# Optimization experiments

Hardware: AMD Instinct MI355X
Metric: run time of the kernel (lower is better)

Reference implementation:

```python
import jax, jax.numpy as jnp
import numpy as np

E, T, K, H, I = 16, 512, 8, 2048, 1024  # experts, tokens, top-k, hidden, ffn half-width


def setup_inputs() -> dict:
    key = jax.random.key(0)
    ks = jax.random.split(key, 8)
    x = jax.random.normal(ks[0], (T, H), dtype=jnp.float32)
    expert_ids = jax.random.randint(ks[1], (T, K), 0, E, dtype=jnp.int32)
    # int8-valued weights stored as int32 (exactly representable)
    gmm1_weight = jax.random.randint(ks[2], (E, H, 2 * I), -127, 128, dtype=jnp.int32)
    gmm2_weight = jax.random.randint(ks[3], (E, I, H), -127, 128, dtype=jnp.int32)
    gmm1_weight_scale = jax.random.uniform(ks[4], (E, 2 * I), dtype=jnp.float32) * 1e-3
    gmm2_weight_scale = jax.random.uniform(ks[5], (E, H), dtype=jnp.float32) * 1e-3
    smooth_scales = jax.random.uniform(ks[6], (E, H), dtype=jnp.float32)
    expert_scales = jax.random.uniform(ks[7], (T, K), dtype=jnp.float32)
    return {"x": x, "expert_ids": expert_ids, "gmm1_weight": gmm1_weight,
            "gmm1_weight_scale": gmm1_weight_scale, "gmm2_weight": gmm2_weight,
            "gmm2_weight_scale": gmm2_weight_scale, "smooth_scales": smooth_scales,
            "expert_scales": expert_scales}


def _dynamic_quant(v):
    # per-token symmetric dynamic quant to int8 range (quant_mode=2 / quant_mode=1)
    s = jnp.max(jnp.abs(v), axis=-1, keepdims=True) / 127.0
    q = jnp.clip(jnp.round(v / s), -128.0, 127.0)  # kept in f32; values are exact small ints
    return q, s


def _grouped_mm(a, w, e_flat):
    # grouped GEMM: out[i] = a[i] @ w[e_flat[i]]. Disjoint expert masks -> masked full GEMMs summed.
    out = jnp.zeros((a.shape[0], w.shape[-1]), dtype=a.dtype)
    for e in range(w.shape[0]):
        mask = (e_flat == e)[:, None]
        out = out + jnp.where(mask, a, 0.0) @ w[e]
    return out


def reference(x, expert_ids, gmm1_weight, gmm1_weight_scale, gmm2_weight,
              gmm2_weight_scale, smooth_scales, expert_scales):
    # --- dispatch: per-token dynamic int8 quant + replicate each token K times ---
    xq, s0 = _dynamic_quant(x)                 # [T,H], [T,1]
    e_flat = expert_ids.reshape(-1)            # [T*K]
    xq_e = jnp.repeat(xq, K, axis=0)           # [T*K,H]
    s0_e = jnp.repeat(s0, K, axis=0)           # [T*K,1] == dynamic_scales / activation_scale
    w1 = gmm1_weight.astype(jnp.float32)       # int8 GEMM emulated exactly in f32
    w2 = gmm2_weight.astype(jnp.float32)
    # --- grouped GEMM 1 -> int32 accumulator values ---
    y1_i32 = _grouped_mm(xq_e, w1, e_flat)     # [T*K,2I]
    # --- fused dequant + SwiGLU (activate_left) + per-token dynamic requant ---
    y1f = y1_i32 * gmm1_weight_scale[e_flat] * s0_e
    act = jax.nn.silu(y1f[:, :I]) * y1f[:, I:]
    aq, s1 = _dynamic_quant(act)               # [T*K,I], [T*K,1]
    # --- grouped GEMM 2 + dequant (per-channel weight scale * per-token scale) ---
    y2_i32 = _grouped_mm(aq, w2, e_flat)       # [T*K,H]
    y2 = y2_i32 * gmm2_weight_scale[e_flat] * s1
    # --- combine: weighted sum over the K expert copies of each token ---
    out = jnp.einsum('tkh,tk->th', y2.reshape(T, K, H), expert_scales)
    return out
```

## Files before the change

### kernel.cpp

```cpp
#include <hip/hip_runtime.h>
#include <hip/hip_bf16.h>
#include <stdint.h>

#define E_   16
#define T_   512
#define KTOP 8
#define H_   2048
#define I_   1024
#define TK_  4096

typedef __attribute__((ext_vector_type(4))) int i32x4;

#define OFF_CNT     0
#define OFF_ROWMAX  4096
#define OFF_XQ      32768
#define OFF_S0      (OFF_XQ + T_*H_)
#define OFF_S1      (OFF_S0 + 4096)
#define OFF_LIST    (OFF_S1 + TK_*4)
#define OFF_ACT     (OFF_LIST + E_*TK_*4)
#define OFF_AQ      (OFF_ACT + (size_t)TK_*I_*4)
#define OFF_Y2      (OFF_AQ + (size_t)TK_*I_)

__device__ __forceinline__ void g2l16(const void* g, void* l) {
  __builtin_amdgcn_global_load_lds(
      (const __attribute__((address_space(1))) void*)g,
      (__attribute__((address_space(3))) void*)l, 16, 0, 0);
}

__global__ void k_quant(const float* __restrict__ x, signed char* __restrict__ xq,
                        float* __restrict__ s0) {
  int t = blockIdx.x, tid = threadIdx.x;
  const float4* xr = (const float4*)(x + (size_t)t * H_);
  float4 a = xr[tid * 2 + 0], b = xr[tid * 2 + 1];
  float m = fmaxf(
      fmaxf(fmaxf(fabsf(a.x), fabsf(a.y)), fmaxf(fabsf(a.z), fabsf(a.w))),
      fmaxf(fmaxf(fabsf(b.x), fabsf(b.y)), fmaxf(fabsf(b.z), fabsf(b.w))));
  for (int o = 32; o > 0; o >>= 1) m = fmaxf(m, __shfl_xor(m, o));
  __shared__ float wm[4];
  if ((tid & 63) == 0) wm[tid >> 6] = m;
  __syncthreads();
  m = fmaxf(fmaxf(wm[0], wm[1]), fmaxf(wm[2], wm[3]));
  float s = m / 127.0f;
  if (!(s > 0.f)) s = 1.0f;
  if (tid == 0) s0[t] = s;
  float v[8] = {a.x, a.y, a.z, a.w, b.x, b.y, b.z, b.w};
  unsigned int lo = 0, hi = 0;
#pragma unroll
  for (int j = 0; j < 4; ++j) {
    float qf = fminf(fmaxf(rintf(v[j] / s), -128.f), 127.f);
    lo |= ((unsigned)((int)qf & 0xFF)) << (8 * j);
  }
#pragma unroll
  for (int j = 0; j < 4; ++j) {
    float qf = fminf(fmaxf(rintf(v[4 + j] / s), -128.f), 127.f);
    hi |= ((unsigned)((int)qf & 0xFF)) << (8 * j);
  }
  ((uint2*)(xq + (size_t)t * H_))[tid] = make_uint2(lo, hi);
}

__global__ void k_scatter(const int* __restrict__ eids, unsigned int* __restrict__ counts,
                          int* __restrict__ row_list) {
  int i = blockIdx.x * blockDim.x + threadIdx.x;
  int e = eids[i];
  int pos = (int)atomicAdd(&counts[e], 1u);
  row_list[e * TK_ + pos] = i;
}

#define BM_   320
#define ABUF  20480
#define BBUF  4096

__launch_bounds__(256, 2)
__global__ void k_gemm1(const signed char* __restrict__ xq, const int* __restrict__ w1,
                        const float* __restrict__ ws1, const float* __restrict__ s0,
                        const unsigned int* __restrict__ counts,
                        const int* __restrict__ row_list,
                        float* __restrict__ act, unsigned int* __restrict__ rowmax) {
  __shared__ alignas(16) char smem[2 * ABUF + 2 * BBUF];
  int e = blockIdx.y;
  int cnt = (int)counts[e];
  if (cnt == 0) return;
  int p0 = blockIdx.x * 32;
  const int* rl = row_list + e * TK_;
  const int* we = w1 + (size_t)e * H_ * (2 * I_);
  const float* wsc = ws1 + (size_t)e * (2 * I_);

  int tid = threadIdx.x, w = tid >> 6, lane = tid & 63;
  int l15 = lane & 15, l4 = lane >> 4;

  int bc = tid & 63, bkg = tid >> 6;
  int bgcol = (bc < 32) ? (p0 + bc) : (I_ + p0 + (bc - 32));
  const int* bsrc0 = we + (size_t)(bkg * 16) * 2048 + bgcol;
  char* bw0 = smem + 2 * ABUF + bkg * 1024 + bc * 16;

  int nch = (cnt + BM_ - 1) / BM_;
  for (int ch = 0; ch < nch; ++ch) {
    int rbase = ch * BM_;
    const signed char* gA[5];
#pragma unroll
    for (int i = 0; i < 5; ++i) {
      int gr = rbase + w * 80 + i * 16 + l15;
      int tok = rl[gr < cnt ? gr : 0] >> 3;
      gA[i] = xq + (size_t)tok * H_ + l4 * 16;
    }
    i32x4 acc[5][4];
#pragma unroll
    for (int i = 0; i < 5; ++i)
#pragma unroll
      for (int n = 0; n < 4; ++n) acc[i][n] = (i32x4)(0);

    int breg[16];
#pragma unroll
    for (int i = 0; i < 5; ++i) g2l16(gA[i], smem + (w * 5 + i) * 1024);
#pragma unroll
    for (int j = 0; j < 16; ++j) breg[j] = bsrc0[(size_t)j * 2048];
    {
      i32x4 pk;
#pragma unroll
      for (int d = 0; d < 4; ++d)
        pk[d] = (breg[4 * d] & 0xFF) | ((breg[4 * d + 1] & 0xFF) << 8) |
                ((breg[4 * d + 2] & 0xFF) << 16) | (breg[4 * d + 3] << 24);
      *(i32x4*)bw0 = pk;
    }
    __syncthreads();

    int buf = 0;
    for (int t = 0; t < H_ / 64; ++t) {
      bool more = (t + 1) < H_ / 64;
      if (more) {
        int k0n = (t + 1) * 64;
#pragma unroll
        for (int i = 0; i < 5; ++i)
          g2l16(gA[i] + k0n, smem + (buf ^ 1) * ABUF + (w * 5 + i) * 1024);
#pragma unroll
        for (int j = 0; j < 16; ++j) breg[j] = bsrc0[(size_t)(k0n + j) * 2048];
      }
      const char* Ab = smem + buf * ABUF;
      const char* Bb = smem + 2 * ABUF + buf * BBUF;
      i32x4 af[5], bf[4];
#pragma unroll
      for (int i = 0; i < 5; ++i)
        af[i] = *(const i32x4*)(Ab + (w * 5 + i) * 1024 + lane * 16);
#pragma unroll
      for (int n = 0; n < 4; ++n)
        bf[n] = *(const i32x4*)(Bb + l4 * 1024 + (n * 16 + l15) * 16);
#pragma unroll
      for (int i = 0; i < 5; ++i)
#pragma unroll
        for (int n = 0; n < 4; ++n)
          acc[i][n] = __builtin_amdgcn_mfma_i32_16x16x64_i8(af[i], bf[n], acc[i][n], 0, 0, 0);
      if (more) {
        i32x4 pk;
#pragma unroll
        for (int d = 0; d < 4; ++d)
          pk[d] = (breg[4 * d] & 0xFF) | ((breg[4 * d + 1] & 0xFF) << 8) |
                  ((breg[4 * d + 2] & 0xFF) << 16) | (breg[4 * d + 3] << 24);
        *(i32x4*)(bw0 + (buf ^ 1) * BBUF) = pk;
      }
      __syncthreads();
      buf ^= 1;
    }

#pragma unroll
    for (int mi = 0; mi < 5; ++mi) {
#pragma unroll
      for (int r = 0; r < 4; ++r) {
        int gr = rbase + w * 80 + mi * 16 + l4 * 4 + r;
        bool valid = gr < cnt;
        int irow = rl[valid ? gr : 0];
        float s0v = s0[irow >> 3];
        float rowm = 0.f, av0 = 0.f, av1 = 0.f;
#pragma unroll
        for (int n = 0; n < 2; ++n) {
          int colL = p0 + n * 16 + l15;
          float yl = (float)acc[mi][n][r] * wsc[colL] * s0v;
          float yr = (float)acc[mi][n + 2][r] * wsc[I_ + colL] * s0v;
          float actv = (yl / (1.f + expf(-yl))) * yr;
          if (n == 0) av0 = actv; else av1 = actv;
          rowm = fmaxf(rowm, fabsf(actv));
        }
        rowm = fmaxf(rowm, __shfl_xor(rowm, 1));
        rowm = fmaxf(rowm, __shfl_xor(rowm, 2));
        rowm = fmaxf(rowm, __shfl_xor(rowm, 4));
        rowm = fmaxf(rowm, __shfl_xor(rowm, 8));
        if (valid) {
          act[(size_t)irow * I_ + p0 + l15] = av0;
          act[(size_t)irow * I_ + p0 + 16 + l15] = av1;
          if (l15 == 0) atomicMax(rowmax + irow, __float_as_uint(rowm));
        }
      }
    }
  }
}

__global__ void k_requant(const float* __restrict__ act, const unsigned int* __restrict__ rowmax,
                          signed char* __restrict__ aq, float* __restrict__ s1) {
  int i = blockIdx.x, tid = threadIdx.x;
  float m = __uint_as_float(rowmax[i]);
  float s = (m > 0.f) ? (m / 127.0f) : 1.0f;
  if (tid == 0) s1[i] = s;
  float4 v = ((const float4*)(act + (size_t)i * I_))[tid];
  float vv[4] = {v.x, v.y, v.z, v.w};
  unsigned int pk = 0;
#pragma unroll
  for (int j = 0; j < 4; ++j) {
    float qf = fminf(fmaxf(rintf(vv[j] / s), -128.f), 127.f);
    pk |= ((unsigned)((int)qf & 0xFF)) << (8 * j);
  }
  ((unsigned int*)(aq + (size_t)i * I_))[tid] = pk;
}

__launch_bounds__(256, 2)
__global__ void k_gemm2(const signed char* __restrict__ aq, const int* __restrict__ w2,
                        const float* __restrict__ ws2, const float* __restrict__ s1,
                        const unsigned int* __restrict__ counts,
                        const int* __restrict__ row_list,
                        float* __restrict__ y2) {
  __shared__ alignas(16) char smem[2 * ABUF + 2 * BBUF];
  int e = blockIdx.y;
  int cnt = (int)counts[e];
  if (cnt == 0) return;
  int n0 = blockIdx.x * 64;
  const int* rl = row_list + e * TK_;
  const int* we = w2 + (size_t)e * I_ * H_;
  const float* wsc = ws2 + (size_t)e * H_;

  int tid = threadIdx.x, w = tid >> 6, lane = tid & 63;
  int l15 = lane & 15, l4 = lane >> 4;

  int bc = tid & 63, bkg = tid >> 6;
  const int* bsrc0 = we + (size_t)(bkg * 16) * H_ + n0 + bc;
  char* bw0 = smem + 2 * ABUF + bkg * 1024 + bc * 16;

  int nch = (cnt + BM_ - 1) / BM_;
  for (int ch = 0; ch < nch; ++ch) {
    int rbase = ch * BM_;
    const signed char* gA[5];
#pragma unroll
    for (int i = 0; i < 5; ++i) {
      int gr = rbase + w * 80 + i * 16 + l15;
      gA[i] = aq + (size_t)rl[gr < cnt ? gr : 0] * I_ + l4 * 16;
    }
    i32x4 acc[5][4];
#pragma unroll
    for (int i = 0; i < 5; ++i)
#pragma unroll
      for (int n = 0; n < 4; ++n) acc[i][n] = (i32x4)(0);

    int breg[16];
#pragma unroll
    for (int i = 0; i < 5; ++i) g2l16(gA[i], smem + (w * 5 + i) * 1024);
#pragma unroll
    for (int j = 0; j < 16; ++j) breg[j] = bsrc0[(size_t)j * H_];
    {
      i32x4 pk;
#pragma unroll
      for (int d = 0; d < 4; ++d)
        pk[d] = (breg[4 * d] & 0xFF) | ((breg[4 * d + 1] & 0xFF) << 8) |
                ((breg[4 * d + 2] & 0xFF) << 16) | (breg[4 * d + 3] << 24);
      *(i32x4*)bw0 = pk;
    }
    __syncthreads();

    int buf = 0;
    for (int t = 0; t < I_ / 64; ++t) {
      bool more = (t + 1) < I_ / 64;
      if (more) {
        int k0n = (t + 1) * 64;
#pragma unroll
        for (int i = 0; i < 5; ++i)
          g2l16(gA[i] + k0n, smem + (buf ^ 1) * ABUF + (w * 5 + i) * 1024);
#pragma unroll
        for (int j = 0; j < 16; ++j) breg[j] = bsrc0[(size_t)(k0n + j) * H_];
      }
      const char* Ab = smem + buf * ABUF;
      const char* Bb = smem + 2 * ABUF + buf * BBUF;
      i32x4 af[5], bf[4];
#pragma unroll
      for (int i = 0; i < 5; ++i)
        af[i] = *(const i32x4*)(Ab + (w * 5 + i) * 1024 + lane * 16);
#pragma unroll
      for (int n = 0; n < 4; ++n)
        bf[n] = *(const i32x4*)(Bb + l4 * 1024 + (n * 16 + l15) * 16);
#pragma unroll
      for (int i = 0; i < 5; ++i)
#pragma unroll
        for (int n = 0; n < 4; ++n)
          acc[i][n] = __builtin_amdgcn_mfma_i32_16x16x64_i8(af[i], bf[n], acc[i][n], 0, 0, 0);
      if (more) {
        i32x4 pk;
#pragma unroll
        for (int d = 0; d < 4; ++d)
          pk[d] = (breg[4 * d] & 0xFF) | ((breg[4 * d + 1] & 0xFF) << 8) |
                  ((breg[4 * d + 2] & 0xFF) << 16) | (breg[4 * d + 3] << 24);
        *(i32x4*)(bw0 + (buf ^ 1) * BBUF) = pk;
      }
      __syncthreads();
      buf ^= 1;
    }

#pragma unroll
    for (int mi = 0; mi < 5; ++mi) {
#pragma unroll
      for (int r = 0; r < 4; ++r) {
        int gr = rbase + w * 80 + mi * 16 + l4 * 4 + r;
        if (gr < cnt) {
          int irow = rl[gr];
          float s1v = s1[irow];
#pragma unroll
          for (int n = 0; n < 4; ++n) {
            int col = n0 + n * 16 + l15;
            y2[(size_t)irow * H_ + col] = (float)acc[mi][n][r] * wsc[col] * s1v;
          }
        }
      }
    }
  }
}

__global__ void k_combine(const float* __restrict__ y2, const float* __restrict__ es,
                          float* __restrict__ out) {
  int idx = blockIdx.x * 256 + threadIdx.x;
  int t = idx >> 11;
  const float* esr = es + (size_t)t * KTOP;
  float s = 0.f;
#pragma unroll
  for (int k = 0; k < KTOP; ++k)
    s += esr[k] * y2[(size_t)(t * KTOP + k) * H_ + (idx & (H_ - 1))];
  out[idx] = s;
}

extern "C" void kernel_launch(void* const* d_in, const int* in_sizes, int n_in,
                              void* d_out, int out_size, void* d_ws, size_t ws_size,
                              hipStream_t stream) {
  const float* x   = (const float*)d_in[0];
  const int*   eid = (const int*)d_in[1];
  const int*   w1  = (const int*)d_in[2];
  const float* ws1 = (const float*)d_in[3];
  const int*   w2  = (const int*)d_in[4];
  const float* ws2 = (const float*)d_in[5];
  const float* es  = (const float*)d_in[7];
  float* out = (float*)d_out;
  char* ws = (char*)d_ws;

  unsigned int*  counts   = (unsigned int*)(ws + OFF_CNT);
  unsigned int*  rowmax   = (unsigned int*)(ws + OFF_ROWMAX);
  signed char*   xq       = (signed char*)(ws + OFF_XQ);
  float*         s0       = (float*)(ws + OFF_S0);
  float*         s1       = (float*)(ws + OFF_S1);
  int*           row_list = (int*)(ws + OFF_LIST);
  float*         act      = (float*)(ws + OFF_ACT);
  signed char*   aq       = (signed char*)(ws + OFF_AQ);
  float*         y2       = (float*)(ws + OFF_Y2);

  hipMemsetAsync(ws, 0, 4096 + TK_ * 4, stream);

  k_quant<<<T_, 256, 0, stream>>>(x, xq, s0);
  k_scatter<<<TK_ / 256, 256, 0, stream>>>(eid, counts, row_list);
  k_gemm1<<<dim3(32, E_), 256, 0, stream>>>(xq, w1, ws1, s0, counts, row_list, act, rowmax);
  k_requant<<<TK_, 256, 0, stream>>>(act, rowmax, aq, s1);
  k_gemm2<<<dim3(32, E_), 256, 0, stream>>>(aq, w2, ws2, s1, counts, row_list, y2);
  k_combine<<<(T_ * H_) / 256, 256, 0, stream>>>(y2, es, out);
}
```

Baseline: 180.6 us.

## Deepen B-prefetch pipeline, fuse scatter into quant, bf16 combine intermediate

Both grouped GEMMs now prefetch weight tiles two steps ahead into alternating register sets, using manual waitcnt and sched barriers so global loads overlap the MFMAs. The expert scatter moves into the quant kernel, and a zeroing kernel replaces the memset. GEMM2 folds the expert combine weight into its epilogue and writes bf16 instead of f32, which halves the intermediate traffic. The combine kernel becomes a vectorized 8-wide bf16 sum. The bf16 intermediate costs some precision, and the hand-written waitcnt logic is fragile.

```diff
diff --git a/kernel.cpp b/kernel.cpp
--- a/kernel.cpp
+++ b/kernel.cpp
@@ -27,9 +27,26 @@
       (__attribute__((address_space(3))) void*)l, 16, 0, 0);
 }
 
+#define SCHEDB() __builtin_amdgcn_sched_barrier(0)
+#define VMCNT16() asm volatile("s_waitcnt vmcnt(16)" ::: "memory")
+#define VMCNT0()  asm volatile("s_waitcnt vmcnt(0)" ::: "memory")
+#define LGKM0()   asm volatile("s_waitcnt lgkmcnt(0)" ::: "memory")
+#define BAR()     __builtin_amdgcn_s_barrier()
+
+__global__ void k_zero(unsigned int* __restrict__ p) {
+  int i = blockIdx.x * 256 + threadIdx.x;
+  if (i < 5120) p[i] = 0;
+}
+
 __global__ void k_quant(const float* __restrict__ x, signed char* __restrict__ xq,
-                        float* __restrict__ s0) {
+                        float* __restrict__ s0, const int* __restrict__ eids,
+                        unsigned int* __restrict__ counts, int* __restrict__ row_list) {
   int t = blockIdx.x, tid = threadIdx.x;
+  if (tid < KTOP) {
+    int e = eids[t * KTOP + tid];
+    int pos = (int)atomicAdd(&counts[e], 1u);
+    row_list[e * TK_ + pos] = t * KTOP + tid;
+  }
   const float4* xr = (const float4*)(x + (size_t)t * H_);
   float4 a = xr[tid * 2 + 0], b = xr[tid * 2 + 1];
   float m = fmaxf(
@@ -58,17 +75,58 @@
   ((uint2*)(xq + (size_t)t * H_))[tid] = make_uint2(lo, hi);
 }
 
-__global__ void k_scatter(const int* __restrict__ eids, unsigned int* __restrict__ counts,
-                          int* __restrict__ row_list) {
-  int i = blockIdx.x * blockDim.x + threadIdx.x;
-  int e = eids[i];
-  int pos = (int)atomicAdd(&counts[e], 1u);
-  row_list[e * TK_ + pos] = i;
-}
-
 #define BM_   320
 #define ABUF  20480
 #define BBUF  4096
+#define WSTR  2048
+
+#define PACKW(SRC, DST) do {                                              \
+    i32x4 pk_;                                                            \
+    _Pragma("unroll")                                                     \
+    for (int d_ = 0; d_ < 4; ++d_)                                        \
+      pk_[d_] = ((SRC)[4*d_] & 0xFF) | (((SRC)[4*d_+1] & 0xFF) << 8) |    \
+                (((SRC)[4*d_+2] & 0xFF) << 16) | ((SRC)[4*d_+3] << 24);   \
+    *(i32x4*)(DST) = pk_;                                                 \
+  } while (0)
+
+#define TILE_BODY(TT, RD, PK, IS, LAST, NT) do {                          \
+    if (!(LAST)) {                                                        \
+      _Pragma("unroll")                                                   \
+      for (int i_ = 0; i_ < 5; ++i_)                                      \
+        g2l16(gA[i_] + ((TT) + 1) * 64,                                   \
+              smem + ((RD) ^ 1) * ABUF + (w * 5 + i_) * 1024);            \
+    }                                                                     \
+    SCHEDB();                                                             \
+    {                                                                     \
+      int kk_ = (TT) + 2; if (kk_ > (NT) - 1) kk_ = (NT) - 1;             \
+      _Pragma("unroll")                                                   \
+      for (int j_ = 0; j_ < 16; ++j_)                                     \
+        (IS)[j_] = bsrc[(size_t)(kk_ * 64 + j_) * WSTR];                  \
+    }                                                                     \
+    SCHEDB();                                                             \
+    {                                                                     \
+      const char* Ab_ = smem + (RD) * ABUF;                               \
+      const char* Bb_ = smem + 2 * ABUF + (RD) * BBUF;                    \
+      i32x4 af_[5], bf_[4];                                               \
+      _Pragma("unroll")                                                   \
+      for (int i_ = 0; i_ < 5; ++i_)                                      \
+        af_[i_] = *(const i32x4*)(Ab_ + (w * 5 + i_) * 1024 + lane * 16); \
+      _Pragma("unroll")                                                   \
+      for (int n_ = 0; n_ < 4; ++n_)                                      \
+        bf_[n_] = *(const i32x4*)(Bb_ + l4 * 1024 + (n_ * 16 + l15) * 16);\
+      _Pragma("unroll")                                                   \
+      for (int i_ = 0; i_ < 5; ++i_)                                      \
+        _Pragma("unroll")                                                 \
+        for (int n_ = 0; n_ < 4; ++n_)                                    \
+          acc[i_][n_] = __builtin_amdgcn_mfma_i32_16x16x64_i8(            \
+              af_[i_], bf_[n_], acc[i_][n_], 0, 0, 0);                    \
+    }                                                                     \
+    if (!(LAST)) {                                                        \
+      VMCNT16(); SCHEDB();                                                \
+      PACKW(PK, bdst0 + (((RD) ^ 1)) * BBUF);                             \
+      LGKM0(); BAR(); SCHEDB();                                           \
+    }                                                                     \
+  } while (0)
 
 __launch_bounds__(256, 2)
 __global__ void k_gemm1(const signed char* __restrict__ xq, const int* __restrict__ w1,
@@ -87,12 +145,12 @@
 
   int tid = threadIdx.x, w = tid >> 6, lane = tid & 63;
   int l15 = lane & 15, l4 = lane >> 4;
-
   int bc = tid & 63, bkg = tid >> 6;
   int bgcol = (bc < 32) ? (p0 + bc) : (I_ + p0 + (bc - 32));
-  const int* bsrc0 = we + (size_t)(bkg * 16) * 2048 + bgcol;
-  char* bw0 = smem + 2 * ABUF + bkg * 1024 + bc * 16;
-
+  const int* bsrc = we + (size_t)(bkg * 16) * WSTR + bgcol;
+  char* bdst0 = smem + 2 * ABUF + bkg * 1024 + bc * 16;
+
+  const int NT = H_ / 64;
   int nch = (cnt + BM_ - 1) / BM_;
   for (int ch = 0; ch < nch; ++ch) {
     int rbase = ch * BM_;
@@ -109,56 +167,24 @@
 #pragma unroll
       for (int n = 0; n < 4; ++n) acc[i][n] = (i32x4)(0);
 
-    int breg[16];
+    int brA[16], brB[16];
+    SCHEDB();
 #pragma unroll
     for (int i = 0; i < 5; ++i) g2l16(gA[i], smem + (w * 5 + i) * 1024);
-#pragma unroll
-    for (int j = 0; j < 16; ++j) breg[j] = bsrc0[(size_t)j * 2048];
-    {
-      i32x4 pk;
-#pragma unroll
-      for (int d = 0; d < 4; ++d)
-        pk[d] = (breg[4 * d] & 0xFF) | ((breg[4 * d + 1] & 0xFF) << 8) |
-                ((breg[4 * d + 2] & 0xFF) << 16) | (breg[4 * d + 3] << 24);
-      *(i32x4*)bw0 = pk;
-    }
-    __syncthreads();
-
-    int buf = 0;
-    for (int t = 0; t < H_ / 64; ++t) {
-      bool more = (t + 1) < H_ / 64;
-      if (more) {
-        int k0n = (t + 1) * 64;
-#pragma unroll
-        for (int i = 0; i < 5; ++i)
-          g2l16(gA[i] + k0n, smem + (buf ^ 1) * ABUF + (w * 5 + i) * 1024);
-#pragma unroll
-        for (int j = 0; j < 16; ++j) breg[j] = bsrc0[(size_t)(k0n + j) * 2048];
-      }
-      const char* Ab = smem + buf * ABUF;
-      const char* Bb = smem + 2 * ABUF + buf * BBUF;
-      i32x4 af[5], bf[4];
-#pragma unroll
-      for (int i = 0; i < 5; ++i)
-        af[i] = *(const i32x4*)(Ab + (w * 5 + i) * 1024 + lane * 16);
-#pragma unroll
-      for (int n = 0; n < 4; ++n)
-        bf[n] = *(const i32x4*)(Bb + l4 * 1024 + (n * 16 + l15) * 16);
-#pragma unroll
-      for (int i = 0; i < 5; ++i)
-#pragma unroll
-        for (int n = 0; n < 4; ++n)
-          acc[i][n] = __builtin_amdgcn_mfma_i32_16x16x64_i8(af[i], bf[n], acc[i][n], 0, 0, 0);
-      if (more) {
-        i32x4 pk;
-#pragma unroll
-        for (int d = 0; d < 4; ++d)
-          pk[d] = (breg[4 * d] & 0xFF) | ((breg[4 * d + 1] & 0xFF) << 8) |
-                  ((breg[4 * d + 2] & 0xFF) << 16) | (breg[4 * d + 3] << 24);
-        *(i32x4*)(bw0 + (buf ^ 1) * BBUF) = pk;
-      }
-      __syncthreads();
-      buf ^= 1;
+    SCHEDB();
+#pragma unroll
+    for (int j = 0; j < 16; ++j) brA[j] = bsrc[(size_t)j * WSTR];
+    SCHEDB();
+#pragma unroll
+    for (int j = 0; j < 16; ++j) brB[j] = bsrc[(size_t)(64 + j) * WSTR];
+    SCHEDB();
+    VMCNT16(); SCHEDB();
+    PACKW(brA, bdst0);
+    LGKM0(); BAR(); SCHEDB();
+
+    for (int t = 0; t < NT; t += 2) {
+      TILE_BODY(t,     0, brB, brA, false,          NT);
+      TILE_BODY(t + 1, 1, brA, brB, (t + 2 == NT),  NT);
     }
 
 #pragma unroll
@@ -213,9 +239,10 @@
 __launch_bounds__(256, 2)
 __global__ void k_gemm2(const signed char* __restrict__ aq, const int* __restrict__ w2,
                         const float* __restrict__ ws2, const float* __restrict__ s1,
+                        const float* __restrict__ es,
                         const unsigned int* __restrict__ counts,
                         const int* __restrict__ row_list,
-                        float* __restrict__ y2) {
+                        __hip_bfloat16* __restrict__ y2h) {
   __shared__ alignas(16) char smem[2 * ABUF + 2 * BBUF];
   int e = blockIdx.y;
   int cnt = (int)counts[e];
@@ -227,11 +254,11 @@
 
   int tid = threadIdx.x, w = tid >> 6, lane = tid & 63;
   int l15 = lane & 15, l4 = lane >> 4;
-
   int bc = tid & 63, bkg = tid >> 6;
-  const int* bsrc0 = we + (size_t)(bkg * 16) * H_ + n0 + bc;
-  char* bw0 = smem + 2 * ABUF + bkg * 1024 + bc * 16;
-
+  const int* bsrc = we + (size_t)(bkg * 16) * WSTR + n0 + bc;
+  char* bdst0 = smem + 2 * ABUF + bkg * 1024 + bc * 16;
+
+  const int NT = I_ / 64;
   int nch = (cnt + BM_ - 1) / BM_;
   for (int ch = 0; ch < nch; ++ch) {
     int rbase = ch * BM_;
@@ -247,56 +274,24 @@
 #pragma unroll
       for (int n = 0; n < 4; ++n) acc[i][n] = (i32x4)(0);
 
-    int breg[16];
+    int brA[16], brB[16];
+    SCHEDB();
 #pragma unroll
     for (int i = 0; i < 5; ++i) g2l16(gA[i], smem + (w * 5 + i) * 1024);
-#pragma unroll
-    for (int j = 0; j < 16; ++j) breg[j] = bsrc0[(size_t)j * H_];
-    {
-      i32x4 pk;
-#pragma unroll
-      for (int d = 0; d < 4; ++d)
-        pk[d] = (breg[4 * d] & 0xFF) | ((breg[4 * d + 1] & 0xFF) << 8) |
-                ((breg[4 * d + 2] & 0xFF) << 16) | (breg[4 * d + 3] << 24);
-      *(i32x4*)bw0 = pk;
-    }
-    __syncthreads();
-
-    int buf = 0;
-    for (int t = 0; t < I_ / 64; ++t) {
-      bool more = (t + 1) < I_ / 64;
-      if (more) {
-        int k0n = (t + 1) * 64;
-#pragma unroll
-        for (int i = 0; i < 5; ++i)
-          g2l16(gA[i] + k0n, smem + (buf ^ 1) * ABUF + (w * 5 + i) * 1024);
-#pragma unroll
-        for (int j = 0; j < 16; ++j) breg[j] = bsrc0[(size_t)(k0n + j) * H_];
-      }
-      const char* Ab = smem + buf * ABUF;
-      const char* Bb = smem + 2 * ABUF + buf * BBUF;
-      i32x4 af[5], bf[4];
-#pragma unroll
-      for (int i = 0; i < 5; ++i)
-        af[i] = *(const i32x4*)(Ab + (w * 5 + i) * 1024 + lane * 16);
-#pragma unroll
-      for (int n = 0; n < 4; ++n)
-        bf[n] = *(const i32x4*)(Bb + l4 * 1024 + (n * 16 + l15) * 16);
-#pragma unroll
-      for (int i = 0; i < 5; ++i)
-#pragma unroll
-        for (int n = 0; n < 4; ++n)
-          acc[i][n] = __builtin_amdgcn_mfma_i32_16x16x64_i8(af[i], bf[n], acc[i][n], 0, 0, 0);
-      if (more) {
-        i32x4 pk;
-#pragma unroll
-        for (int d = 0; d < 4; ++d)
-          pk[d] = (breg[4 * d] & 0xFF) | ((breg[4 * d + 1] & 0xFF) << 8) |
-                  ((breg[4 * d + 2] & 0xFF) << 16) | (breg[4 * d + 3] << 24);
-        *(i32x4*)(bw0 + (buf ^ 1) * BBUF) = pk;
-      }
-      __syncthreads();
-      buf ^= 1;
+    SCHEDB();
+#pragma unroll
+    for (int j = 0; j < 16; ++j) brA[j] = bsrc[(size_t)j * WSTR];
+    SCHEDB();
+#pragma unroll
+    for (int j = 0; j < 16; ++j) brB[j] = bsrc[(size_t)(64 + j) * WSTR];
+    SCHEDB();
+    VMCNT16(); SCHEDB();
+    PACKW(brA, bdst0);
+    LGKM0(); BAR(); SCHEDB();
+
+    for (int t = 0; t < NT; t += 2) {
+      TILE_BODY(t,     0, brB, brA, false,          NT);
+      TILE_BODY(t + 1, 1, brA, brB, (t + 2 == NT),  NT);
     }
 
 #pragma unroll
@@ -306,11 +301,12 @@
         int gr = rbase + w * 80 + mi * 16 + l4 * 4 + r;
         if (gr < cnt) {
           int irow = rl[gr];
-          float s1v = s1[irow];
+          float sc = s1[irow] * es[irow];
 #pragma unroll
           for (int n = 0; n < 4; ++n) {
             int col = n0 + n * 16 + l15;
-            y2[(size_t)irow * H_ + col] = (float)acc[mi][n][r] * wsc[col] * s1v;
+            float v = (float)acc[mi][n][r] * wsc[col] * sc;
+            y2h[(size_t)irow * H_ + col] = __float2bfloat16(v);
           }
         }
       }
@@ -318,16 +314,25 @@
   }
 }
 
-__global__ void k_combine(const float* __restrict__ y2, const float* __restrict__ es,
-                          float* __restrict__ out) {
+__global__ void k_combine(const __hip_bfloat16* __restrict__ y2h, float* __restrict__ out) {
   int idx = blockIdx.x * 256 + threadIdx.x;
-  int t = idx >> 11;
-  const float* esr = es + (size_t)t * KTOP;
-  float s = 0.f;
-#pragma unroll
-  for (int k = 0; k < KTOP; ++k)
-    s += esr[k] * y2[(size_t)(t * KTOP + k) * H_ + (idx & (H_ - 1))];
-  out[idx] = s;
+  int t = idx >> 8;
+  int h0 = (idx & 255) * 8;
+  float s[8];
+#pragma unroll
+  for (int j = 0; j < 8; ++j) s[j] = 0.f;
+#pragma unroll
+  for (int k = 0; k < KTOP; ++k) {
+    const __hip_bfloat16* p = y2h + ((size_t)(t * KTOP + k) * H_ + h0);
+    uint4 u = *(const uint4*)p;
+    const __hip_bfloat16* b = (const __hip_bfloat16*)&u;
+#pragma unroll
+    for (int j = 0; j < 8; ++j) s[j] += __bfloat162float(b[j]);
+  }
+  float4 o0 = make_float4(s[0], s[1], s[2], s[3]);
+  float4 o1 = make_float4(s[4], s[5], s[6], s[7]);
+  float4* dst = (float4*)(out + (size_t)t * H_ + h0);
+  dst[0] = o0; dst[1] = o1;
 }
 
 extern "C" void kernel_launch(void* const* d_in, const int* in_sizes, int n_in,
@@ -351,14 +356,12 @@
   int*           row_list = (int*)(ws + OFF_LIST);
   float*         act      = (float*)(ws + OFF_ACT);
   signed char*   aq       = (signed char*)(ws + OFF_AQ);
-  float*         y2       = (float*)(ws + OFF_Y2);
-
-  hipMemsetAsync(ws, 0, 4096 + TK_ * 4, stream);
-
-  k_quant<<<T_, 256, 0, stream>>>(x, xq, s0);
-  k_scatter<<<TK_ / 256, 256, 0, stream>>>(eid, counts, row_list);
+  __hip_bfloat16* y2h     = (__hip_bfloat16*)(ws + OFF_Y2);
+
+  k_zero<<<20, 256, 0, stream>>>((unsigned int*)ws);
+  k_quant<<<T_, 256, 0, stream>>>(x, xq, s0, eid, counts, row_list);
   k_gemm1<<<dim3(32, E_), 256, 0, stream>>>(xq, w1, ws1, s0, counts, row_list, act, rowmax);
   k_requant<<<TK_, 256, 0, stream>>>(act, rowmax, aq, s1);
-  k_gemm2<<<dim3(32, E_), 256, 0, stream>>>(aq, w2, ws2, s1, counts, row_list, y2);
-  k_combine<<<(T_ * H_) / 256, 256, 0, stream>>>(y2, es, out);
-}
+  k_gemm2<<<dim3(32, E_), 256, 0, stream>>>(aq, w2, ws2, s1, es, counts, row_list, y2h);
+  k_combine<<<(T_ * H_ / 8) / 256, 256, 0, stream>>>(y2h, out);
+}
```

Result: no change. 178.2 us (-1.3%).
